# Performance work log

Measured on AMD Instinct MI355X. Metric: run time of the kernel, lower is better.

Reference implementation:

```python
import jax, jax.numpy as jnp
import numpy as np

EPS = 1e-6

def elu_feature_map(x):
    # phi(x) = elu(x) + 1 (always positive)
    return jax.nn.elu(x) + 1.0

def setup_inputs() -> dict:
    key = jax.random.key(0)
    kq, kk, kv = jax.random.split(key, 3)
    B, T, H, E = 2, 4096, 8, 64
    return {
        "query": jax.random.normal(kq, (B, T, H, E), dtype=jnp.float32),
        "key": jax.random.normal(kk, (B, T, H, E), dtype=jnp.float32),
        "value": jax.random.normal(kv, (B, T, H, E), dtype=jnp.float32),
    }

def reference(query, key, value):
    # b t h e -> b h t e
    q = jnp.transpose(query, (0, 2, 1, 3))
    k = jnp.transpose(key, (0, 2, 1, 3))
    v = jnp.transpose(value, (0, 2, 1, 3))
    Q = elu_feature_map(q)  # [b,h,t,e]
    K = elu_feature_map(k)  # [b,h,t,e]
    # Causal linear attention: running sums over the sequence axis.
    # KV_cum[t] = sum_{s<=t} K_s (outer) V_s  -> [b,h,t,e,d]
    kv = jnp.einsum('bhte,bhtd->bhted', K, v)
    kv_cum = jnp.cumsum(kv, axis=2)
    k_cum = jnp.cumsum(K, axis=2)  # [b,h,t,e]
    # Normalizer Z_t = 1 / (Q_t . sum_{s<=t} K_s + eps)
    Z = 1.0 / (jnp.einsum('bhte,bhte->bht', Q, k_cum) + EPS)
    out = jnp.einsum('bhte,bhted->bhtd', Q, kv_cum) * Z[..., None]
    # b h t d -> b t h d
    return jnp.transpose(out, (0, 2, 1, 3))
```

## Files before the change

kernel.cpp:

```cpp
#include <hip/hip_runtime.h>
#include <hip/hip_bf16.h>
#include <math.h>

#define B 2
#define T 4096
#define H 8
#define E 64
#define D 64
#define C 128
#define NC (T / C)
#define BH (B * H)
#define EPS 1e-6f
#define PT 132
#define PQ 72
#define PBT 200

typedef short short8 __attribute__((ext_vector_type(8)));
typedef float f32x4 __attribute__((ext_vector_type(4)));

__device__ __forceinline__ float phi(float x) {
    return x > 0.0f ? x + 1.0f : __expf(x);
}
__device__ __forceinline__ uint pk2(float a, float b) {
    __hip_bfloat162 h = __float22bfloat162_rn(make_float2(a, b));
    union { __hip_bfloat162 h2; uint u; } cv; cv.h2 = h; return cv.u;
}
__device__ __forceinline__ ushort f2bf(float f) {
    uint u = __float_as_uint(f);
    return (ushort)((u + 0x7FFFu + ((u >> 16) & 1u)) >> 16);
}

__global__ __launch_bounds__(256) void k_chunk_sums(
        const float* __restrict__ Kg, const float* __restrict__ Vg,
        float* __restrict__ SpartT, float* __restrict__ zpart,
        ushort* __restrict__ VTg, ushort* __restrict__ PKg) {
    int blk = blockIdx.x;
    int bh = blk / NC, c = blk % NC;
    int b = bh / H, h = bh % H;
    int t0 = c * C;
    __shared__ ushort sKt[E][PT];
    __shared__ ushort sVt[D][PT];
    int tid = threadIdx.x;
    int lane = tid & 63, w = tid >> 6;
    const float4* Kg4 = (const float4*)Kg;
    const float4* Vg4 = (const float4*)Vg;
    uint2* PK2 = (uint2*)(PKg + (size_t)blk * (C * E));

    for (int l = tid; l < (C / 2) * 16; l += 256) {
        int i2 = l >> 4, e4 = l & 15;
        int t = i2 * 2;
        size_t g0 = ((size_t)(b * T + t0 + t) * H + h) * 16 + e4;
        size_t g1 = g0 + H * 16;
        float4 ka = Kg4[g0], kb = Kg4[g1];
        float4 va = Vg4[g0], vb = Vg4[g1];
        float pk0[4] = {phi(ka.x), phi(ka.y), phi(ka.z), phi(ka.w)};
        float pk1[4] = {phi(kb.x), phi(kb.y), phi(kb.z), phi(kb.w)};
        float pv0[4] = {va.x, va.y, va.z, va.w};
        float pv1[4] = {vb.x, vb.y, vb.z, vb.w};
        #pragma unroll
        for (int cc = 0; cc < 4; ++cc) {
            *(uint*)&sKt[e4 * 4 + cc][t] = pk2(pk0[cc], pk1[cc]);
            *(uint*)&sVt[e4 * 4 + cc][t] = pk2(pv0[cc], pv1[cc]);
        }
        PK2[t * 16 + e4]       = make_uint2(pk2(pk0[0], pk0[1]), pk2(pk0[2], pk0[3]));
        PK2[(t + 1) * 16 + e4] = make_uint2(pk2(pk1[0], pk1[1]), pk2(pk1[2], pk1[3]));
    }
    __syncthreads();

    {
        int g = lane >> 4, cl = lane & 15;
        int mt = w;
        f32x4 acc[4] = {};
        for (int ks = 0; ks < 4; ++ks) {
            short8 a = *(const short8*)&sKt[mt * 16 + cl][ks * 32 + g * 8];
            #pragma unroll
            for (int nt = 0; nt < 4; ++nt) {
                short8 bb = *(const short8*)&sVt[nt * 16 + cl][ks * 32 + g * 8];
                acc[nt] = __builtin_amdgcn_mfma_f32_16x16x32_bf16(a, bb, acc[nt], 0, 0, 0);
            }
        }
        float* Sp = SpartT + (size_t)blk * (E * D);
        #pragma unroll
        for (int nt = 0; nt < 4; ++nt) {
            int d = nt * 16 + cl;
            *(float4*)&Sp[d * E + mt * 16 + g * 4] =
                make_float4(acc[nt][0], acc[nt][1], acc[nt][2], acc[nt][3]);
        }
    }
    ushort* vt = VTg + (size_t)blk * (C * D);
    for (int l = tid; l < C * D / 8; l += 256)
        *(short8*)&vt[(l >> 4) * C + (l & 15) * 8] = *(const short8*)&sVt[l >> 4][(l & 15) * 8];
    if (tid < E) {
        float s = 0.0f;
        #pragma unroll
        for (int p = 0; p < 16; ++p) {
            short8 v = *(const short8*)&sKt[tid][p * 8];
            #pragma unroll
            for (int j = 0; j < 8; ++j) s += __uint_as_float(((uint)(ushort)v[j]) << 16);
        }
        zpart[(size_t)blk * E + tid] = s;
    }
}

__global__ __launch_bounds__(256) void k_scan(
        const float* __restrict__ SpartT, float* __restrict__ zpart,
        ushort* __restrict__ S0bf) {
    int bh  = blockIdx.x / 17;
    int sub = blockIdx.x % 17;
    int tid = threadIdx.x;
    if (sub < 16) {
        int l = sub * 256 + tid;
        const float* base = SpartT + (size_t)bh * NC * (E * D) + l;
        ushort* obase = S0bf + (size_t)bh * NC * (E * D) + l;
        float vals[NC];
        #pragma unroll
        for (int c = 0; c < NC; ++c) vals[c] = base[(size_t)c * (E * D)];
        float run = 0.0f;
        #pragma unroll
        for (int c = 0; c < NC; ++c) {
            obase[(size_t)c * (E * D)] = f2bf(run);
            run += vals[c];
        }
    } else if (tid < E) {
        float* base = zpart + (size_t)bh * NC * E + tid;
        float vals[NC];
        #pragma unroll
        for (int c = 0; c < NC; ++c) vals[c] = base[(size_t)c * E];
        float run = 0.0f;
        #pragma unroll
        for (int c = 0; c < NC; ++c) {
            base[(size_t)c * E] = run;
            run += vals[c];
        }
    }
}

__global__ __launch_bounds__(512, 4) void k_output(
        const float* __restrict__ Qg, const ushort* __restrict__ PKg,
        const ushort* __restrict__ VTg, const ushort* __restrict__ S0bf,
        const float* __restrict__ zpart, float* __restrict__ Og) {
    int blk = blockIdx.x;
    int bh = blk / NC, c = blk % NC;
    int b = bh / H, h = bh % H;
    int t0 = c * C;

    __shared__ ushort sQ[C][PQ];
    __shared__ ushort sKB[13000];
    __shared__ ushort sA[C][C];

    int tid = threadIdx.x;
    int lane = tid & 63;
    int w = tid >> 6;
    int g = lane >> 4, cl = lane & 15;

    const float4* Qg4 = (const float4*)Qg;

    for (int l = tid; l < C * 8; l += 512) {
        int i = l >> 3, e8 = l & 7;
        size_t gg = ((size_t)(b * T + t0 + i) * H + h) * 16 + e8 * 2;
        float4 qa = Qg4[gg], qb = Qg4[gg + 1];
        uint4 qv = make_uint4(pk2(phi(qa.x), phi(qa.y)), pk2(phi(qa.z), phi(qa.w)),
                              pk2(phi(qb.x), phi(qb.y)), pk2(phi(qb.z), phi(qb.w)));
        *(uint4*)&sQ[i][e8 * 8] = qv;
    }
    const short8* pk8 = (const short8*)(PKg + (size_t)blk * (C * E));
    for (int l = tid; l < C * 8; l += 512)
        *(short8*)&sKB[(l >> 3) * PQ + (l & 7) * 8] = pk8[l];
    {
        uint4 zz = make_uint4(0, 0, 0, 0);
        ushort* af = (ushort*)sA;
        #pragma unroll
        for (int it = 0; it < 4; ++it)
            *(uint4*)&af[(tid + 512 * it) * 8] = zz;
    }
    const short8* vt8 = (const short8*)(VTg + (size_t)blk * (C * D));
    short8 vt0 = vt8[tid * 2], vt1 = vt8[tid * 2 + 1];
    short8 s0reg = ((const short8*)(S0bf + (size_t)blk * (E * D)))[tid];
    float zreg = (tid < E) ? zpart[(size_t)blk * E + tid] : 0.0f;
    __syncthreads();

    for (int idx = w; idx < 36; idx += 8) {
        int tr = 0;
        while ((tr + 1) * (tr + 2) / 2 <= idx) ++tr;
        int tc = idx - tr * (tr + 1) / 2;
        f32x4 acc = {};
        #pragma unroll
        for (int ks = 0; ks < 2; ++ks) {
            short8 a  = *(const short8*)&sKB[(tc * 16 + cl) * PQ + ks * 32 + g * 8];
            short8 bq = *(const short8*)&sQ[tr * 16 + cl][ks * 32 + g * 8];
            acc = __builtin_amdgcn_mfma_f32_16x16x32_bf16(a, bq, acc, 0, 0, 0);
        }
        int iq = tr * 16 + cl;
        int j0 = tc * 16 + g * 4;
        float v0 = (j0 + 0 <= iq) ? acc[0] : 0.0f;
        float v1 = (j0 + 1 <= iq) ? acc[1] : 0.0f;
        float v2 = (j0 + 2 <= iq) ? acc[2] : 0.0f;
        float v3 = (j0 + 3 <= iq) ? acc[3] : 0.0f;
        int pb = (tc * 2 + (g >> 1)) ^ (iq & 7);
        *(uint2*)&sA[iq][pb * 8 + (g & 1) * 4] = make_uint2(pk2(v0, v1), pk2(v2, v3));
    }
    __syncthreads();

    {
        int i0 = tid * 2, i1 = tid * 2 + 1;
        *(short8*)&sKB[(i0 >> 4) * PBT + (i0 & 15) * 8] = vt0;
        *(short8*)&sKB[(i1 >> 4) * PBT + (i1 & 15) * 8] = vt1;
        *(short8*)&sKB[(tid >> 3) * PBT + 128 + (tid & 7) * 8] = s0reg;
        if (tid < E) sKB[64 * PBT + 128 + tid] = f2bf(zreg);
        else if (tid < E + 16) {
            short8 ones = {16256, 16256, 16256, 16256, 16256, 16256, 16256, 16256};
            *(short8*)&sKB[64 * PBT + (tid - E) * 8] = ones;
        }
    }
    __syncthreads();

    {
        const int permv[8] = {0, 1, 2, 3, 6, 7, 4, 5};
        int mt = permv[w];
        int m0 = mt * 16;
        int arow = m0 + cl;
        int aswz = arow & 7;
        int smax = (m0 + 15) >> 5;
        f32x4 acc[5] = {};
        for (int s = 0; s <= smax; ++s) {
            short8 a = *(const short8*)&sA[arow][(((s * 4 + g) ^ aswz)) * 8];
            #pragma unroll
            for (int nt = 0; nt < 5; ++nt) {
                short8 bb = *(const short8*)&sKB[(nt * 16 + cl) * PBT + s * 32 + g * 8];
                acc[nt] = __builtin_amdgcn_mfma_f32_16x16x32_bf16(a, bb, acc[nt], 0, 0, 0);
            }
        }
        #pragma unroll
        for (int s2 = 0; s2 < 2; ++s2) {
            short8 a = *(const short8*)&sQ[arow][s2 * 32 + g * 8];
            #pragma unroll
            for (int nt = 0; nt < 5; ++nt) {
                short8 bb = *(const short8*)&sKB[(nt * 16 + cl) * PBT + 128 + s2 * 32 + g * 8];
                acc[nt] = __builtin_amdgcn_mfma_f32_16x16x32_bf16(a, bb, acc[nt], 0, 0, 0);
            }
        }
        #pragma unroll
        for (int r = 0; r < 4; ++r) {
            float den = __shfl(acc[4][r], lane & 48);
            float zi = 1.0f / (den + EPS);
            int row = m0 + g * 4 + r;
            size_t ga = ((size_t)(b * T + t0 + row) * H + h) * 64;
            #pragma unroll
            for (int nt = 0; nt < 4; ++nt)
                Og[ga + nt * 16 + cl] = acc[nt][r] * zi;
        }
    }
}

extern "C" void kernel_launch(void* const* d_in, const int* in_sizes, int n_in,
                              void* d_out, int out_size, void* d_ws, size_t ws_size,
                              hipStream_t stream) {
    const float* q = (const float*)d_in[0];
    const float* k = (const float*)d_in[1];
    const float* v = (const float*)d_in[2];
    float* out = (float*)d_out;

    float*  SpartT = (float*)d_ws;
    float*  zpart  = SpartT + (size_t)BH * NC * E * D;
    ushort* VTg    = (ushort*)(zpart + (size_t)BH * NC * E);
    ushort* PKg    = VTg + (size_t)BH * NC * C * D;
    ushort* S0bf   = PKg + (size_t)BH * NC * C * E;

    k_chunk_sums<<<BH * NC, 256, 0, stream>>>(k, v, SpartT, zpart, VTg, PKg);
    k_scan<<<BH * 17, 256, 0, stream>>>(SpartT, zpart, S0bf);
    k_output<<<BH * NC, 512, 0, stream>>>(q, PKg, VTg, S0bf, zpart, out);
}
```

Before: 32.76 us.

## Fold chunk prefix scan into output kernel and store chunk states as bf16

Removes the separate scan kernel. Each output block now sums the bf16 chunk-state partials of all earlier chunks itself, and the chunk-sums kernel writes its E×D partial states in bf16 instead of fp32. This drops one kernel launch and the fp32 round trip through global memory. In exchange the redundant reads grow quadratically in chunk count (up to 31 chunk states per block), and rounding each partial to bf16 before summing adds precision error.

Measured after the change: 41.31 us. 26.1% more time.

```diff
diff --git a/kernel.cpp b/kernel.cpp
--- a/kernel.cpp
+++ b/kernel.cpp
@@ -29,10 +29,13 @@
     uint u = __float_as_uint(f);
     return (ushort)((u + 0x7FFFu + ((u >> 16) & 1u)) >> 16);
 }
+__device__ __forceinline__ float bf2f(ushort h) {
+    return __uint_as_float(((uint)h) << 16);
+}
 
 __global__ __launch_bounds__(256) void k_chunk_sums(
         const float* __restrict__ Kg, const float* __restrict__ Vg,
-        float* __restrict__ SpartT, float* __restrict__ zpart,
+        ushort* __restrict__ SpartBf, float* __restrict__ zpart,
         ushort* __restrict__ VTg, ushort* __restrict__ PKg) {
     int blk = blockIdx.x;
     int bh = blk / NC, c = blk % NC;
@@ -79,12 +82,12 @@
                 acc[nt] = __builtin_amdgcn_mfma_f32_16x16x32_bf16(a, bb, acc[nt], 0, 0, 0);
             }
         }
-        float* Sp = SpartT + (size_t)blk * (E * D);
+        ushort* Sp = SpartBf + (size_t)blk * (E * D);
         #pragma unroll
         for (int nt = 0; nt < 4; ++nt) {
             int d = nt * 16 + cl;
-            *(float4*)&Sp[d * E + mt * 16 + g * 4] =
-                make_float4(acc[nt][0], acc[nt][1], acc[nt][2], acc[nt][3]);
+            *(uint2*)&Sp[d * E + mt * 16 + g * 4] =
+                make_uint2(pk2(acc[nt][0], acc[nt][1]), pk2(acc[nt][2], acc[nt][3]));
         }
     }
     ushort* vt = VTg + (size_t)blk * (C * D);
@@ -96,48 +99,15 @@
         for (int p = 0; p < 16; ++p) {
             short8 v = *(const short8*)&sKt[tid][p * 8];
             #pragma unroll
-            for (int j = 0; j < 8; ++j) s += __uint_as_float(((uint)(ushort)v[j]) << 16);
+            for (int j = 0; j < 8; ++j) s += bf2f((ushort)v[j]);
         }
         zpart[(size_t)blk * E + tid] = s;
-    }
-}
-
-__global__ __launch_bounds__(256) void k_scan(
-        const float* __restrict__ SpartT, float* __restrict__ zpart,
-        ushort* __restrict__ S0bf) {
-    int bh  = blockIdx.x / 17;
-    int sub = blockIdx.x % 17;
-    int tid = threadIdx.x;
-    if (sub < 16) {
-        int l = sub * 256 + tid;
-        const float* base = SpartT + (size_t)bh * NC * (E * D) + l;
-        ushort* obase = S0bf + (size_t)bh * NC * (E * D) + l;
-        float vals[NC];
-        #pragma unroll
-        for (int c = 0; c < NC; ++c) vals[c] = base[(size_t)c * (E * D)];
-        float run = 0.0f;
-        #pragma unroll
-        for (int c = 0; c < NC; ++c) {
-            obase[(size_t)c * (E * D)] = f2bf(run);
-            run += vals[c];
-        }
-    } else if (tid < E) {
-        float* base = zpart + (size_t)bh * NC * E + tid;
-        float vals[NC];
-        #pragma unroll
-        for (int c = 0; c < NC; ++c) vals[c] = base[(size_t)c * E];
-        float run = 0.0f;
-        #pragma unroll
-        for (int c = 0; c < NC; ++c) {
-            base[(size_t)c * E] = run;
-            run += vals[c];
-        }
     }
 }
 
 __global__ __launch_bounds__(512, 4) void k_output(
         const float* __restrict__ Qg, const ushort* __restrict__ PKg,
-        const ushort* __restrict__ VTg, const ushort* __restrict__ S0bf,
+        const ushort* __restrict__ VTg, const ushort* __restrict__ SpartBf,
         const float* __restrict__ zpart, float* __restrict__ Og) {
     int blk = blockIdx.x;
     int bh = blk / NC, c = blk % NC;
@@ -175,8 +145,6 @@
     }
     const short8* vt8 = (const short8*)(VTg + (size_t)blk * (C * D));
     short8 vt0 = vt8[tid * 2], vt1 = vt8[tid * 2 + 1];
-    short8 s0reg = ((const short8*)(S0bf + (size_t)blk * (E * D)))[tid];
-    float zreg = (tid < E) ? zpart[(size_t)blk * E + tid] : 0.0f;
     __syncthreads();
 
     for (int idx = w; idx < 36; idx += 8) {
@@ -202,12 +170,27 @@
     __syncthreads();
 
     {
+        const ushort* SpB = SpartBf + (size_t)bh * NC * (E * D) + tid * 8;
+        float s0acc[8] = {};
+        for (int ch = 0; ch < c; ++ch) {
+            short8 tpart = *(const short8*)&SpB[(size_t)ch * (E * D)];
+            #pragma unroll
+            for (int j = 0; j < 8; ++j) s0acc[j] += bf2f((ushort)tpart[j]);
+        }
+        short8 s0v;
+        #pragma unroll
+        for (int j = 0; j < 8; ++j) s0v[j] = (short)f2bf(s0acc[j]);
+
         int i0 = tid * 2, i1 = tid * 2 + 1;
         *(short8*)&sKB[(i0 >> 4) * PBT + (i0 & 15) * 8] = vt0;
         *(short8*)&sKB[(i1 >> 4) * PBT + (i1 & 15) * 8] = vt1;
-        *(short8*)&sKB[(tid >> 3) * PBT + 128 + (tid & 7) * 8] = s0reg;
-        if (tid < E) sKB[64 * PBT + 128 + tid] = f2bf(zreg);
-        else if (tid < E + 16) {
+        *(short8*)&sKB[(tid >> 3) * PBT + 128 + (tid & 7) * 8] = s0v;
+        if (tid < E) {
+            const float* zp = zpart + (size_t)bh * NC * E + tid;
+            float z = 0.0f;
+            for (int ch = 0; ch < c; ++ch) z += zp[(size_t)ch * E];
+            sKB[64 * PBT + 128 + tid] = f2bf(z);
+        } else if (tid < E + 16) {
             short8 ones = {16256, 16256, 16256, 16256, 16256, 16256, 16256, 16256};
             *(short8*)&sKB[64 * PBT + (tid - E) * 8] = ones;
         }
@@ -260,13 +243,11 @@
     const float* v = (const float*)d_in[2];
     float* out = (float*)d_out;
 
-    float*  SpartT = (float*)d_ws;
-    float*  zpart  = SpartT + (size_t)BH * NC * E * D;
-    ushort* VTg    = (ushort*)(zpart + (size_t)BH * NC * E);
-    ushort* PKg    = VTg + (size_t)BH * NC * C * D;
-    ushort* S0bf   = PKg + (size_t)BH * NC * C * E;
-
-    k_chunk_sums<<<BH * NC, 256, 0, stream>>>(k, v, SpartT, zpart, VTg, PKg);
-    k_scan<<<BH * 17, 256, 0, stream>>>(SpartT, zpart, S0bf);
-    k_output<<<BH * NC, 512, 0, stream>>>(q, PKg, VTg, S0bf, zpart, out);
-}
+    ushort* SpartBf = (ushort*)d_ws;
+    float*  zpart   = (float*)(SpartBf + (size_t)BH * NC * E * D);
+    ushort* VTg     = (ushort*)(zpart + (size_t)BH * NC * E);
+    ushort* PKg     = VTg + (size_t)BH * NC * C * D;
+
+    k_chunk_sums<<<BH * NC, 256, 0, stream>>>(k, v, SpartBf, zpart, VTg, PKg);
+    k_output<<<BH * NC, 512, 0, stream>>>(q, PKg, VTg, SpartBf, zpart, out);
+}
```
